# Performance work log

Measured on AMD Instinct MI355X. Metric: run time of the kernel, lower is better.

Reference implementation:

```python
import jax, jax.numpy as jnp
import numpy as np


def setup_inputs() -> dict:
    key = jax.random.key(0)
    k1, k2, k3, k4 = jax.random.split(key, 4)
    B, N, F, S, OUT = 8, 50000, 32, 16, 64
    x = jax.random.normal(k1, (B, N, F), dtype=jnp.float32)
    spiral_adj = jax.random.randint(k2, (B, N, S), 0, N, dtype=jnp.int64)
    W = jax.random.normal(k3, (OUT, F * S), dtype=jnp.float32) * (1.0 / np.sqrt(F * S))
    b = jax.random.normal(k4, (OUT,), dtype=jnp.float32) * 0.01
    return {"x": x, "spiral_adj": spiral_adj, "W": W, "b": b}


def reference(x, spiral_adj, W, b):
    B, N, F = x.shape
    S = spiral_adj.shape[-1]
    # Per-batch gather of spiral neighbors: (B, N, S, F)
    spirals = jax.vmap(lambda xb, ab: xb[ab])(x, spiral_adj)
    spirals = spirals.reshape(B, N, S * F)
    # Linear: y = spirals @ W^T + b, then ELU
    out = jnp.einsum('bnk,ok->bno', spirals, W) + b
    out = jax.nn.elu(out)
    # zero out the last (padding) vertex
    mask = jnp.ones((1, N, 1), dtype=out.dtype).at[0, -1, 0].set(0.0)
    return out * mask
```

## Files before the change

kernel.cpp:

```cpp
#include <hip/hip_runtime.h>
#include <hip/hip_bf16.h>
#include <string.h>

#define B_ 8
#define N_ 50000
#define F_ 32
#define S_ 16
#define O_ 64
#define K_ (F_ * S_)
#define XELEMS (B_ * N_ * F_)
#define TPB (N_ / 16)
#define BPB 196

typedef __attribute__((ext_vector_type(8))) short bf16x8;
typedef __attribute__((ext_vector_type(4))) float f32x4;
typedef __attribute__((ext_vector_type(4))) int int4v;

union bfpack { bf16x8 v; __hip_bfloat16 h[8]; };

__global__ __launch_bounds__(256) void prep_kernel(const float* __restrict__ W,
                                                   unsigned short* __restrict__ Wb,
                                                   const float* __restrict__ x,
                                                   unsigned short* __restrict__ xb) {
    int bid = blockIdx.x;
    if (bid < 128) {
        int i = bid * 256 + threadIdx.x;
        int j = i & 7;
        int o = (i >> 3) & 63;
        int qk = i >> 9;
        int quad = qk & 3;
        int kt = qk >> 2;
        __hip_bfloat16 h = __float2bfloat16(W[o * K_ + kt * 32 + quad * 8 + j]);
        unsigned short u; memcpy(&u, &h, 2);
        Wb[i] = u;
    } else {
        int i = (bid - 128) * 256 + threadIdx.x;
        if (i < XELEMS / 8) {
            size_t base = (size_t)i * 8;
            f32x4 a = __builtin_nontemporal_load((const f32x4*)(x + base));
            f32x4 b = __builtin_nontemporal_load((const f32x4*)(x + base + 4));
            bfpack p;
            p.h[0] = __float2bfloat16(a[0]); p.h[1] = __float2bfloat16(a[1]);
            p.h[2] = __float2bfloat16(a[2]); p.h[3] = __float2bfloat16(a[3]);
            p.h[4] = __float2bfloat16(b[0]); p.h[5] = __float2bfloat16(b[1]);
            p.h[6] = __float2bfloat16(b[2]); p.h[7] = __float2bfloat16(b[3]);
            *(bf16x8*)(xb + base) = p.v;
        }
    }
}

__global__ __launch_bounds__(256, 2) void spiral_kernel(
        const unsigned short* __restrict__ xb, const int* __restrict__ adj,
        const unsigned short* __restrict__ Wb, const float* __restrict__ bias,
        float* __restrict__ out) {
    const int lane = threadIdx.x & 63;
    const int wv   = threadIdx.x >> 6;
    const int m16  = lane & 15;
    const int quad = lane >> 4;

    const int b  = blockIdx.x & 7;
    const int jb = blockIdx.x >> 3;
    const int tib0 = (jb * 4 + wv) * 4;

    __shared__ __align__(16) unsigned char ring[4][4][4][1024];

    int rowbase[4];
    int nn[4];
#pragma unroll
    for (int vt = 0; vt < 4; ++vt) {
        int t = tib0 + vt;
        if (t >= TPB) t = TPB - 1;
        nn[vt] = t * 16;
        rowbase[vt] = b * N_ + t * 16;
    }
    const size_t xbase = (size_t)b * N_ * F_;

    int4v aj_all[4][4];
#pragma unroll
    for (int vt = 0; vt < 4; ++vt)
#pragma unroll
        for (int kt4 = 0; kt4 < 4; ++kt4)
            aj_all[vt][kt4] = __builtin_nontemporal_load(
                (const int4v*)(adj + (size_t)(rowbase[vt] + m16) * S_ + kt4 * 4));

    f32x4 acc[4][4];
#pragma unroll
    for (int vt = 0; vt < 4; ++vt)
#pragma unroll
        for (int nt = 0; nt < 4; ++nt)
            acc[vt][nt] = (f32x4){0.f, 0.f, 0.f, 0.f};

    bf16x8 wfp[4][4];

#define GATHER_ISSUE(g_)                                                                   \
    do {                                                                                   \
        if ((g_) < 16) {                                                                   \
            const int kt4_ = (g_) >> 2, q_ = (g_) & 3;                                     \
            _Pragma("unroll")                                                              \
            for (int vt = 0; vt < 4; ++vt) {                                               \
                int a_ = aj_all[vt][kt4_][q_];                                             \
                const unsigned short* src_ = xb + xbase + (size_t)a_ * F_ + quad * 8;      \
                __builtin_amdgcn_global_load_lds(                                          \
                    (const __attribute__((address_space(1))) void*)src_,                   \
                    (__attribute__((address_space(3))) void*)&ring[wv][(g_) & 3][vt][0],   \
                    16, 0, 0);                                                             \
            }                                                                              \
        }                                                                                  \
    } while (0)

#define LOAD_W(g_)                                                                         \
    do {                                                                                   \
        if ((g_) < 16) {                                                                   \
            _Pragma("unroll")                                                              \
            for (int nt = 0; nt < 4; ++nt)                                                 \
                wfp[(g_) & 3][nt] = *(const bf16x8*)(                                      \
                    Wb + (size_t)(((g_) * 4 + quad) * 64 + nt * 16 + m16) * 8);            \
        }                                                                                  \
    } while (0)

#define SB __builtin_amdgcn_sched_barrier(0)

    GATHER_ISSUE(0); SB; LOAD_W(0); SB;
    GATHER_ISSUE(1); SB; LOAD_W(1); SB;
    GATHER_ISSUE(2); SB; LOAD_W(2); SB;

#pragma unroll
    for (int g = 0; g < 16; ++g) {
        GATHER_ISSUE(g + 3); SB;
        LOAD_W(g + 3); SB;
        if (g < 13)       asm volatile("s_waitcnt vmcnt(24)" ::: "memory");
        else if (g == 13) asm volatile("s_waitcnt vmcnt(16)" ::: "memory");
        else if (g == 14) asm volatile("s_waitcnt vmcnt(8)"  ::: "memory");
        else              asm volatile("s_waitcnt vmcnt(0)"  ::: "memory");
        SB;
        bf16x8 xf[4];
#pragma unroll
        for (int vt = 0; vt < 4; ++vt)
            xf[vt] = *(const bf16x8*)&ring[wv][g & 3][vt][(size_t)lane * 16];
#pragma unroll
        for (int vt = 0; vt < 4; ++vt)
#pragma unroll
            for (int nt = 0; nt < 4; ++nt)
                acc[vt][nt] = __builtin_amdgcn_mfma_f32_16x16x32_bf16(wfp[g & 3][nt], xf[vt], acc[vt][nt], 0, 0, 0);
        SB;
    }
#undef GATHER_ISSUE
#undef LOAD_W
#undef SB

#pragma unroll
    for (int vt = 0; vt < 4; ++vt) {
        const int n = nn[vt] + m16;
        const bool zero = (n == N_ - 1);
        float* orow = out + (size_t)(rowbase[vt] + m16) * O_ + quad * 4;
#pragma unroll
        for (int nt = 0; nt < 4; ++nt) {
            f32x4 bv = *(const f32x4*)(bias + nt * 16 + quad * 4);
            f32x4 v;
#pragma unroll
            for (int r = 0; r < 4; ++r) {
                float t = acc[vt][nt][r] + bv[r];
                t = t > 0.f ? t : (__expf(t) - 1.f);
                v[r] = zero ? 0.f : t;
            }
            *(f32x4*)(orow + nt * 16) = v;
        }
    }
}

__global__ __launch_bounds__(256) void wconv_kernel(const float* __restrict__ W,
                                                    unsigned short* __restrict__ Wb) {
    int i = blockIdx.x * 256 + threadIdx.x;
    if (i < O_ * K_) {
        int j = i & 7, o = (i >> 3) & 63, qk = i >> 9;
        int quad = qk & 3, kt = qk >> 2;
        __hip_bfloat16 h = __float2bfloat16(W[o * K_ + kt * 32 + quad * 8 + j]);
        unsigned short u; memcpy(&u, &h, 2);
        Wb[i] = u;
    }
}

__global__ __launch_bounds__(256) void spiral_f32_kernel(
        const float* __restrict__ x, const int* __restrict__ adj,
        const unsigned short* __restrict__ Wb, const float* __restrict__ bias,
        float* __restrict__ out) {
    const int lane = threadIdx.x & 63;
    const int wv = threadIdx.x >> 6;
    const int m16 = lane & 15, quad = lane >> 4;
    const int b  = blockIdx.x & 7;
    const int jb = blockIdx.x >> 3;
    const int tib0 = (jb * 4 + wv) * 4;
    int rowbase[4], nn[4];
#pragma unroll
    for (int vt = 0; vt < 4; ++vt) {
        int t = tib0 + vt;
        if (t >= TPB) t = TPB - 1;
        nn[vt] = t * 16;
        rowbase[vt] = b * N_ + t * 16;
    }
    f32x4 acc[4][4];
#pragma unroll
    for (int vt = 0; vt < 4; ++vt)
#pragma unroll
        for (int nt = 0; nt < 4; ++nt) acc[vt][nt] = (f32x4){0.f,0.f,0.f,0.f};
    for (int kt = 0; kt < 16; ++kt) {
        bf16x8 wf[4];
#pragma unroll
        for (int nt = 0; nt < 4; ++nt)
            wf[nt] = *(const bf16x8*)(Wb + (size_t)((kt * 4 + quad) * 64 + nt * 16 + m16) * 8);
#pragma unroll
        for (int vt = 0; vt < 4; ++vt) {
            int a = adj[(size_t)(rowbase[vt] + m16) * S_ + kt];
            const float* xr = x + ((size_t)b * N_ + a) * F_ + quad * 8;
            f32x4 x0 = *(const f32x4*)xr;
            f32x4 x1 = *(const f32x4*)(xr + 4);
            bfpack af;
            af.h[0]=__float2bfloat16(x0[0]); af.h[1]=__float2bfloat16(x0[1]);
            af.h[2]=__float2bfloat16(x0[2]); af.h[3]=__float2bfloat16(x0[3]);
            af.h[4]=__float2bfloat16(x1[0]); af.h[5]=__float2bfloat16(x1[1]);
            af.h[6]=__float2bfloat16(x1[2]); af.h[7]=__float2bfloat16(x1[3]);
#pragma unroll
            for (int nt = 0; nt < 4; ++nt)
                acc[vt][nt] = __builtin_amdgcn_mfma_f32_16x16x32_bf16(wf[nt], af.v, acc[vt][nt], 0, 0, 0);
        }
    }
#pragma unroll
    for (int vt = 0; vt < 4; ++vt) {
        const int n = nn[vt] + m16;
        const bool zero = (n == N_ - 1);
        float* orow = out + (size_t)(rowbase[vt] + m16) * O_ + quad * 4;
#pragma unroll
        for (int nt = 0; nt < 4; ++nt) {
            f32x4 bv = *(const f32x4*)(bias + nt * 16 + quad * 4);
            f32x4 v;
#pragma unroll
            for (int r = 0; r < 4; ++r) {
                float t = acc[vt][nt][r] + bv[r];
                t = t > 0.f ? t : (__expf(t) - 1.f);
                v[r] = zero ? 0.f : t;
            }
            *(f32x4*)(orow + nt * 16) = v;
        }
    }
}

extern "C" void kernel_launch(void* const* d_in, const int* in_sizes, int n_in,
                              void* d_out, int out_size, void* d_ws, size_t ws_size,
                              hipStream_t stream) {
    const float* x    = (const float*)d_in[0];
    const int*   adj  = (const int*)d_in[1];
    const float* W    = (const float*)d_in[2];
    const float* bias = (const float*)d_in[3];
    float* out = (float*)d_out;

    const size_t wb_bytes = (size_t)O_ * K_ * 2;
    const size_t xb_bytes = (size_t)XELEMS * 2;
    unsigned short* Wb = (unsigned short*)d_ws;
    unsigned short* xb = (unsigned short*)((char*)d_ws + wb_bytes);

    const int grid_main = 8 * BPB;

    if (ws_size >= wb_bytes + xb_bytes) {
        int grid_prep = 128 + (XELEMS / 8 + 255) / 256;
        hipLaunchKernelGGL(prep_kernel, dim3(grid_prep), dim3(256), 0, stream, W, Wb, x, xb);
        hipLaunchKernelGGL(spiral_kernel, dim3(grid_main), dim3(256), 0, stream,
                           xb, adj, Wb, bias, out);
    } else {
        hipLaunchKernelGGL(wconv_kernel, dim3(128), dim3(256), 0, stream, W, Wb);
        hipLaunchKernelGGL(spiral_f32_kernel, dim3(grid_main), dim3(256), 0, stream,
                           x, adj, Wb, bias, out);
    }
}
```

Before: 230.5 us.

## Fuse bf16 prep and spiral GEMM into persistent cooperative kernel with atomic tile queue

Merges the W/x bf16 conversion and the gather+MFMA spiral kernel into one cooperative launch of 512 blocks. A grid-wide sync separates the two phases, and blocks then pull tile indices from per-batch atomic counters instead of using a fixed grid mapping. This removes a kernel launch boundary and lets blocks balance work dynamically. In exchange it pays for a grid sync, adds atomic and __syncthreads overhead per tile, and uses fewer resident blocks (512) in the conversion phase. The counters are never reset but are offset by a base value read at kernel start.

```diff
diff --git a/kernel.cpp b/kernel.cpp
--- a/kernel.cpp
+++ b/kernel.cpp
@@ -1,4 +1,5 @@
 #include <hip/hip_runtime.h>
+#include <hip/hip_cooperative_groups.h>
 #include <hip/hip_bf16.h>
 #include <string.h>
 
@@ -11,6 +12,7 @@
 #define XELEMS (B_ * N_ * F_)
 #define TPB (N_ / 16)
 #define BPB 196
+#define GRID_COOP 512
 
 typedef __attribute__((ext_vector_type(8))) short bf16x8;
 typedef __attribute__((ext_vector_type(4))) float f32x4;
@@ -18,54 +20,13 @@
 
 union bfpack { bf16x8 v; __hip_bfloat16 h[8]; };
 
-__global__ __launch_bounds__(256) void prep_kernel(const float* __restrict__ W,
-                                                   unsigned short* __restrict__ Wb,
-                                                   const float* __restrict__ x,
-                                                   unsigned short* __restrict__ xb) {
-    int bid = blockIdx.x;
-    if (bid < 128) {
-        int i = bid * 256 + threadIdx.x;
-        int j = i & 7;
-        int o = (i >> 3) & 63;
-        int qk = i >> 9;
-        int quad = qk & 3;
-        int kt = qk >> 2;
-        __hip_bfloat16 h = __float2bfloat16(W[o * K_ + kt * 32 + quad * 8 + j]);
-        unsigned short u; memcpy(&u, &h, 2);
-        Wb[i] = u;
-    } else {
-        int i = (bid - 128) * 256 + threadIdx.x;
-        if (i < XELEMS / 8) {
-            size_t base = (size_t)i * 8;
-            f32x4 a = __builtin_nontemporal_load((const f32x4*)(x + base));
-            f32x4 b = __builtin_nontemporal_load((const f32x4*)(x + base + 4));
-            bfpack p;
-            p.h[0] = __float2bfloat16(a[0]); p.h[1] = __float2bfloat16(a[1]);
-            p.h[2] = __float2bfloat16(a[2]); p.h[3] = __float2bfloat16(a[3]);
-            p.h[4] = __float2bfloat16(b[0]); p.h[5] = __float2bfloat16(b[1]);
-            p.h[6] = __float2bfloat16(b[2]); p.h[7] = __float2bfloat16(b[3]);
-            *(bf16x8*)(xb + base) = p.v;
-        }
-    }
-}
-
-__global__ __launch_bounds__(256, 2) void spiral_kernel(
+__device__ __forceinline__ void spiral_body(
         const unsigned short* __restrict__ xb, const int* __restrict__ adj,
         const unsigned short* __restrict__ Wb, const float* __restrict__ bias,
-        float* __restrict__ out) {
-    const int lane = threadIdx.x & 63;
-    const int wv   = threadIdx.x >> 6;
-    const int m16  = lane & 15;
-    const int quad = lane >> 4;
-
-    const int b  = blockIdx.x & 7;
-    const int jb = blockIdx.x >> 3;
-    const int tib0 = (jb * 4 + wv) * 4;
-
-    __shared__ __align__(16) unsigned char ring[4][4][4][1024];
-
-    int rowbase[4];
-    int nn[4];
+        float* __restrict__ out, unsigned char* ringw,
+        int b, int tib0, int lane, int m16, int quad)
+{
+    int rowbase[4], nn[4];
 #pragma unroll
     for (int vt = 0; vt < 4; ++vt) {
         int t = tib0 + vt;
@@ -102,7 +63,7 @@
                 const unsigned short* src_ = xb + xbase + (size_t)a_ * F_ + quad * 8;      \
                 __builtin_amdgcn_global_load_lds(                                          \
                     (const __attribute__((address_space(1))) void*)src_,                   \
-                    (__attribute__((address_space(3))) void*)&ring[wv][(g_) & 3][vt][0],   \
+                    (__attribute__((address_space(3))) void*)(ringw + ((((g_) & 3) * 4 + vt) << 10)), \
                     16, 0, 0);                                                             \
             }                                                                              \
         }                                                                                  \
@@ -136,7 +97,7 @@
         bf16x8 xf[4];
 #pragma unroll
         for (int vt = 0; vt < 4; ++vt)
-            xf[vt] = *(const bf16x8*)&ring[wv][g & 3][vt][(size_t)lane * 16];
+            xf[vt] = *(const bf16x8*)(ringw + (((g & 3) * 4 + vt) << 10) + lane * 16);
 #pragma unroll
         for (int vt = 0; vt < 4; ++vt)
 #pragma unroll
@@ -166,6 +127,99 @@
             *(f32x4*)(orow + nt * 16) = v;
         }
     }
+}
+
+__global__ __launch_bounds__(256, 2) void fused_kernel(
+        const float* __restrict__ x, const int* __restrict__ adj,
+        const float* __restrict__ W, const float* __restrict__ bias,
+        float* __restrict__ out, unsigned short* __restrict__ Wb,
+        unsigned short* __restrict__ xb, unsigned int* __restrict__ ctr)
+{
+    __shared__ __align__(16) unsigned char ring[4][4][4][1024];
+    __shared__ unsigned int sh_base, sh_g;
+
+    const int tid = threadIdx.x;
+    const unsigned gid = blockIdx.x * 256u + (unsigned)tid;
+    const int b = blockIdx.x & 7;
+
+    if (tid == 0) sh_base = ctr[b];
+
+    if (gid < (unsigned)(O_ * K_)) {
+        int j = gid & 7, o = (gid >> 3) & 63, qk = gid >> 9;
+        int quad_ = qk & 3, kt = qk >> 2;
+        __hip_bfloat16 h = __float2bfloat16(W[o * K_ + kt * 32 + quad_ * 8 + j]);
+        unsigned short u; memcpy(&u, &h, 2);
+        Wb[gid] = u;
+    }
+    for (unsigned i = gid; i < (unsigned)(XELEMS / 8); i += GRID_COOP * 256u) {
+        size_t base = (size_t)i * 8;
+        f32x4 a = __builtin_nontemporal_load((const f32x4*)(x + base));
+        f32x4 c = __builtin_nontemporal_load((const f32x4*)(x + base + 4));
+        bfpack p;
+        p.h[0] = __float2bfloat16(a[0]); p.h[1] = __float2bfloat16(a[1]);
+        p.h[2] = __float2bfloat16(a[2]); p.h[3] = __float2bfloat16(a[3]);
+        p.h[4] = __float2bfloat16(c[0]); p.h[5] = __float2bfloat16(c[1]);
+        p.h[6] = __float2bfloat16(c[2]); p.h[7] = __float2bfloat16(c[3]);
+        *(bf16x8*)(xb + base) = p.v;
+    }
+    __threadfence();
+    cooperative_groups::this_grid().sync();
+
+    const int lane = tid & 63, wv = tid >> 6;
+    const int m16 = lane & 15, quad = lane >> 4;
+    unsigned char* ringw = &ring[wv][0][0][0];
+
+    for (;;) {
+        __syncthreads();
+        if (tid == 0) sh_g = atomicAdd(&ctr[b], 1u) - sh_base;
+        __syncthreads();
+        unsigned g = sh_g;
+        if (g >= (unsigned)BPB) break;
+        spiral_body(xb, adj, Wb, bias, out, ringw, b, ((int)g * 4 + wv) * 4, lane, m16, quad);
+    }
+}
+
+__global__ __launch_bounds__(256) void prep_kernel(const float* __restrict__ W,
+                                                   unsigned short* __restrict__ Wb,
+                                                   const float* __restrict__ x,
+                                                   unsigned short* __restrict__ xb) {
+    int bid = blockIdx.x;
+    if (bid < 128) {
+        int i = bid * 256 + threadIdx.x;
+        int j = i & 7, o = (i >> 3) & 63, qk = i >> 9;
+        int quad = qk & 3, kt = qk >> 2;
+        __hip_bfloat16 h = __float2bfloat16(W[o * K_ + kt * 32 + quad * 8 + j]);
+        unsigned short u; memcpy(&u, &h, 2);
+        Wb[i] = u;
+    } else {
+        int i = (bid - 128) * 256 + threadIdx.x;
+        if (i < XELEMS / 8) {
+            size_t base = (size_t)i * 8;
+            f32x4 a = __builtin_nontemporal_load((const f32x4*)(x + base));
+            f32x4 c = __builtin_nontemporal_load((const f32x4*)(x + base + 4));
+            bfpack p;
+            p.h[0] = __float2bfloat16(a[0]); p.h[1] = __float2bfloat16(a[1]);
+            p.h[2] = __float2bfloat16(a[2]); p.h[3] = __float2bfloat16(a[3]);
+            p.h[4] = __float2bfloat16(c[0]); p.h[5] = __float2bfloat16(c[1]);
+            p.h[6] = __float2bfloat16(c[2]); p.h[7] = __float2bfloat16(c[3]);
+            *(bf16x8*)(xb + base) = p.v;
+        }
+    }
+}
+
+__global__ __launch_bounds__(256, 2) void spiral_kernel(
+        const unsigned short* __restrict__ xb, const int* __restrict__ adj,
+        const unsigned short* __restrict__ Wb, const float* __restrict__ bias,
+        float* __restrict__ out) {
+    __shared__ __align__(16) unsigned char ring[4][4][4][1024];
+    const int lane = threadIdx.x & 63;
+    const int wv   = threadIdx.x >> 6;
+    const int m16  = lane & 15;
+    const int quad = lane >> 4;
+    const int b  = blockIdx.x & 7;
+    const int jb = blockIdx.x >> 3;
+    spiral_body(xb, adj, Wb, bias, out, &ring[wv][0][0][0],
+                b, (jb * 4 + wv) * 4, lane, m16, quad);
 }
 
 __global__ __launch_bounds__(256) void wconv_kernel(const float* __restrict__ W,
@@ -255,10 +309,22 @@
 
     const size_t wb_bytes = (size_t)O_ * K_ * 2;
     const size_t xb_bytes = (size_t)XELEMS * 2;
+    const size_t ctr_off  = wb_bytes + xb_bytes;
     unsigned short* Wb = (unsigned short*)d_ws;
     unsigned short* xb = (unsigned short*)((char*)d_ws + wb_bytes);
+    unsigned int*  ctr = (unsigned int*)((char*)d_ws + ctr_off);
 
     const int grid_main = 8 * BPB;
+
+    if (ws_size >= ctr_off + 32) {
+        void* args[8] = { (void*)&x, (void*)&adj, (void*)&W, (void*)&bias,
+                          (void*)&out, (void*)&Wb, (void*)&xb, (void*)&ctr };
+        hipError_t e = hipLaunchCooperativeKernel((const void*)fused_kernel,
+                                                  dim3(GRID_COOP), dim3(256),
+                                                  args, 0, stream);
+        if (e == hipSuccess) return;
+        (void)hipGetLastError();
+    }
 
     if (ws_size >= wb_bytes + xb_bytes) {
         int grid_prep = 128 + (XELEMS / 8 + 255) / 256;
```

After: 413.9 us. +79.6%, slower.

## Stage full bf16 weight matrix in LDS once per block instead of per-wave global loads

Applied to the files above, without the earlier changes.

Each block now copies the whole 64 KB bf16 weight matrix into shared memory with async global-to-LDS loads at kernel start. The MFMA loop reads weight fragments from LDS rather than issuing its own global loads, which lowers the vmcnt wait thresholds and frees registers that held the prefetched weights. In exchange, launch bounds drop to one block per CU because of the larger LDS footprint, and there is a block-wide barrier before the main loop. This cuts occupancy and the latency hiding that a second block provided.

```diff
diff --git a/kernel.cpp b/kernel.cpp
--- a/kernel.cpp
+++ b/kernel.cpp
@@ -49,10 +49,13 @@
     }
 }
 
-__global__ __launch_bounds__(256, 2) void spiral_kernel(
+__global__ __launch_bounds__(256, 1) void spiral_kernel(
         const unsigned short* __restrict__ xb, const int* __restrict__ adj,
         const unsigned short* __restrict__ Wb, const float* __restrict__ bias,
         float* __restrict__ out) {
+    __shared__ __align__(16) unsigned short Wlds[32768];
+    __shared__ __align__(16) unsigned char ring[4][4][4][1024];
+
     const int lane = threadIdx.x & 63;
     const int wv   = threadIdx.x >> 6;
     const int m16  = lane & 15;
@@ -62,10 +65,9 @@
     const int jb = blockIdx.x >> 3;
     const int tib0 = (jb * 4 + wv) * 4;
 
-    __shared__ __align__(16) unsigned char ring[4][4][4][1024];
-
-    int rowbase[4];
-    int nn[4];
+    unsigned char* ringw = &ring[wv][0][0][0];
+
+    int rowbase[4], nn[4];
 #pragma unroll
     for (int vt = 0; vt < 4; ++vt) {
         int t = tib0 + vt;
@@ -75,6 +77,18 @@
     }
     const size_t xbase = (size_t)b * N_ * F_;
 
+#define SB __builtin_amdgcn_sched_barrier(0)
+
+#pragma unroll
+    for (int i = 0; i < 16; ++i) {
+        const unsigned short* src = Wb + (((size_t)wv * 16 + i) << 9) + lane * 8;
+        __builtin_amdgcn_global_load_lds(
+            (const __attribute__((address_space(1))) void*)src,
+            (__attribute__((address_space(3))) void*)((unsigned char*)Wlds + (((wv * 16 + i)) << 10)),
+            16, 0, 0);
+    }
+    SB;
+
     int4v aj_all[4][4];
 #pragma unroll
     for (int vt = 0; vt < 4; ++vt)
@@ -82,6 +96,7 @@
         for (int kt4 = 0; kt4 < 4; ++kt4)
             aj_all[vt][kt4] = __builtin_nontemporal_load(
                 (const int4v*)(adj + (size_t)(rowbase[vt] + m16) * S_ + kt4 * 4));
+    SB;
 
     f32x4 acc[4][4];
 #pragma unroll
@@ -89,8 +104,6 @@
 #pragma unroll
         for (int nt = 0; nt < 4; ++nt)
             acc[vt][nt] = (f32x4){0.f, 0.f, 0.f, 0.f};
-
-    bf16x8 wfp[4][4];
 
 #define GATHER_ISSUE(g_)                                                                   \
     do {                                                                                   \
@@ -102,50 +115,41 @@
                 const unsigned short* src_ = xb + xbase + (size_t)a_ * F_ + quad * 8;      \
                 __builtin_amdgcn_global_load_lds(                                          \
                     (const __attribute__((address_space(1))) void*)src_,                   \
-                    (__attribute__((address_space(3))) void*)&ring[wv][(g_) & 3][vt][0],   \
+                    (__attribute__((address_space(3))) void*)(ringw + ((((g_) & 3) * 4 + vt) << 10)), \
                     16, 0, 0);                                                             \
             }                                                                              \
         }                                                                                  \
     } while (0)
 
-#define LOAD_W(g_)                                                                         \
-    do {                                                                                   \
-        if ((g_) < 16) {                                                                   \
-            _Pragma("unroll")                                                              \
-            for (int nt = 0; nt < 4; ++nt)                                                 \
-                wfp[(g_) & 3][nt] = *(const bf16x8*)(                                      \
-                    Wb + (size_t)(((g_) * 4 + quad) * 64 + nt * 16 + m16) * 8);            \
-        }                                                                                  \
-    } while (0)
-
-#define SB __builtin_amdgcn_sched_barrier(0)
-
-    GATHER_ISSUE(0); SB; LOAD_W(0); SB;
-    GATHER_ISSUE(1); SB; LOAD_W(1); SB;
-    GATHER_ISSUE(2); SB; LOAD_W(2); SB;
+    GATHER_ISSUE(0); SB;
+    GATHER_ISSUE(1); SB;
+    GATHER_ISSUE(2); SB;
+    asm volatile("s_waitcnt vmcnt(12)" ::: "memory");
+    __syncthreads();
 
 #pragma unroll
     for (int g = 0; g < 16; ++g) {
         GATHER_ISSUE(g + 3); SB;
-        LOAD_W(g + 3); SB;
-        if (g < 13)       asm volatile("s_waitcnt vmcnt(24)" ::: "memory");
-        else if (g == 13) asm volatile("s_waitcnt vmcnt(16)" ::: "memory");
-        else if (g == 14) asm volatile("s_waitcnt vmcnt(8)"  ::: "memory");
+        if (g < 13)       asm volatile("s_waitcnt vmcnt(12)" ::: "memory");
+        else if (g == 13) asm volatile("s_waitcnt vmcnt(8)"  ::: "memory");
+        else if (g == 14) asm volatile("s_waitcnt vmcnt(4)"  ::: "memory");
         else              asm volatile("s_waitcnt vmcnt(0)"  ::: "memory");
         SB;
-        bf16x8 xf[4];
+        bf16x8 xf[4], wf[4];
 #pragma unroll
         for (int vt = 0; vt < 4; ++vt)
-            xf[vt] = *(const bf16x8*)&ring[wv][g & 3][vt][(size_t)lane * 16];
+            xf[vt] = *(const bf16x8*)(ringw + (((g & 3) * 4 + vt) << 10) + lane * 16);
+#pragma unroll
+        for (int nt = 0; nt < 4; ++nt)
+            wf[nt] = *(const bf16x8*)(Wlds + (size_t)((g * 4 + quad) * 64 + nt * 16 + m16) * 8);
 #pragma unroll
         for (int vt = 0; vt < 4; ++vt)
 #pragma unroll
             for (int nt = 0; nt < 4; ++nt)
-                acc[vt][nt] = __builtin_amdgcn_mfma_f32_16x16x32_bf16(wfp[g & 3][nt], xf[vt], acc[vt][nt], 0, 0, 0);
+                acc[vt][nt] = __builtin_amdgcn_mfma_f32_16x16x32_bf16(wf[nt], xf[vt], acc[vt][nt], 0, 0, 0);
         SB;
     }
 #undef GATHER_ISSUE
-#undef LOAD_W
 #undef SB
 
 #pragma unroll
```

Result: no change. 232.8 us (+1.0%).

## Convert spiral kernel to persistent grid with per-batch atomic work counters

Applied to the files above, without the earlier changes.

Replaces the fixed 1568-block launch with 512 persistent blocks. Each block repeatedly grabs a tile index from a per-batch atomic counter, and the counters are zeroed in the prep kernel. The goal is to cut block launch and tail overhead and balance the load across CUs. In exchange it adds two barriers and an atomic per tile, and it loses the overlap of the prologue and epilogue between tiles that independent blocks had.

```diff
diff --git a/kernel.cpp b/kernel.cpp
--- a/kernel.cpp
+++ b/kernel.cpp
@@ -11,6 +11,7 @@
 #define XELEMS (B_ * N_ * F_)
 #define TPB (N_ / 16)
 #define BPB 196
+#define GRID_PERS 512
 
 typedef __attribute__((ext_vector_type(8))) short bf16x8;
 typedef __attribute__((ext_vector_type(4))) float f32x4;
@@ -21,8 +22,10 @@
 __global__ __launch_bounds__(256) void prep_kernel(const float* __restrict__ W,
                                                    unsigned short* __restrict__ Wb,
                                                    const float* __restrict__ x,
-                                                   unsigned short* __restrict__ xb) {
+                                                   unsigned short* __restrict__ xb,
+                                                   unsigned int* __restrict__ ctr) {
     int bid = blockIdx.x;
+    if (bid == 0 && threadIdx.x < 8) ctr[threadIdx.x] = 0u;
     if (bid < 128) {
         int i = bid * 256 + threadIdx.x;
         int j = i & 7;
@@ -49,23 +52,13 @@
     }
 }
 
-__global__ __launch_bounds__(256, 2) void spiral_kernel(
+__device__ __forceinline__ void spiral_body(
         const unsigned short* __restrict__ xb, const int* __restrict__ adj,
         const unsigned short* __restrict__ Wb, const float* __restrict__ bias,
-        float* __restrict__ out) {
-    const int lane = threadIdx.x & 63;
-    const int wv   = threadIdx.x >> 6;
-    const int m16  = lane & 15;
-    const int quad = lane >> 4;
-
-    const int b  = blockIdx.x & 7;
-    const int jb = blockIdx.x >> 3;
-    const int tib0 = (jb * 4 + wv) * 4;
-
-    __shared__ __align__(16) unsigned char ring[4][4][4][1024];
-
-    int rowbase[4];
-    int nn[4];
+        float* __restrict__ out, unsigned char* ringw,
+        int b, int tib0, int lane, int m16, int quad)
+{
+    int rowbase[4], nn[4];
 #pragma unroll
     for (int vt = 0; vt < 4; ++vt) {
         int t = tib0 + vt;
@@ -102,7 +95,7 @@
                 const unsigned short* src_ = xb + xbase + (size_t)a_ * F_ + quad * 8;      \
                 __builtin_amdgcn_global_load_lds(                                          \
                     (const __attribute__((address_space(1))) void*)src_,                   \
-                    (__attribute__((address_space(3))) void*)&ring[wv][(g_) & 3][vt][0],   \
+                    (__attribute__((address_space(3))) void*)(ringw + ((((g_) & 3) * 4 + vt) << 10)), \
                     16, 0, 0);                                                             \
             }                                                                              \
         }                                                                                  \
@@ -136,7 +129,7 @@
         bf16x8 xf[4];
 #pragma unroll
         for (int vt = 0; vt < 4; ++vt)
-            xf[vt] = *(const bf16x8*)&ring[wv][g & 3][vt][(size_t)lane * 16];
+            xf[vt] = *(const bf16x8*)(ringw + (((g & 3) * 4 + vt) << 10) + lane * 16);
 #pragma unroll
         for (int vt = 0; vt < 4; ++vt)
 #pragma unroll
@@ -165,6 +158,33 @@
             }
             *(f32x4*)(orow + nt * 16) = v;
         }
+    }
+}
+
+__global__ __launch_bounds__(256, 2) void spiral_kernel(
+        const unsigned short* __restrict__ xb, const int* __restrict__ adj,
+        const unsigned short* __restrict__ Wb, const float* __restrict__ bias,
+        float* __restrict__ out, unsigned int* __restrict__ ctr) {
+    __shared__ __align__(16) unsigned char ring[4][4][4][1024];
+    __shared__ unsigned int sh_g;
+
+    const int tid  = threadIdx.x;
+    const int lane = tid & 63;
+    const int wv   = tid >> 6;
+    const int m16  = lane & 15;
+    const int quad = lane >> 4;
+    const int b    = blockIdx.x & 7;
+
+    unsigned char* ringw = &ring[wv][0][0][0];
+
+    for (;;) {
+        __syncthreads();
+        if (tid == 0) sh_g = atomicAdd(&ctr[b], 1u);
+        __syncthreads();
+        const unsigned g = sh_g;
+        if (g >= (unsigned)BPB) break;
+        spiral_body(xb, adj, Wb, bias, out, ringw,
+                    b, ((int)g * 4 + wv) * 4, lane, m16, quad);
     }
 }
 
@@ -255,19 +275,20 @@
 
     const size_t wb_bytes = (size_t)O_ * K_ * 2;
     const size_t xb_bytes = (size_t)XELEMS * 2;
+    const size_t ctr_off  = wb_bytes + xb_bytes;
     unsigned short* Wb = (unsigned short*)d_ws;
     unsigned short* xb = (unsigned short*)((char*)d_ws + wb_bytes);
-
-    const int grid_main = 8 * BPB;
-
-    if (ws_size >= wb_bytes + xb_bytes) {
+    unsigned int*  ctr = (unsigned int*)((char*)d_ws + ctr_off);
+
+    if (ws_size >= ctr_off + 32) {
         int grid_prep = 128 + (XELEMS / 8 + 255) / 256;
-        hipLaunchKernelGGL(prep_kernel, dim3(grid_prep), dim3(256), 0, stream, W, Wb, x, xb);
-        hipLaunchKernelGGL(spiral_kernel, dim3(grid_main), dim3(256), 0, stream,
-                           xb, adj, Wb, bias, out);
+        hipLaunchKernelGGL(prep_kernel, dim3(grid_prep), dim3(256), 0, stream,
+                           W, Wb, x, xb, ctr);
+        hipLaunchKernelGGL(spiral_kernel, dim3(GRID_PERS), dim3(256), 0, stream,
+                           xb, adj, Wb, bias, out, ctr);
     } else {
         hipLaunchKernelGGL(wconv_kernel, dim3(128), dim3(256), 0, stream, W, Wb);
-        hipLaunchKernelGGL(spiral_f32_kernel, dim3(grid_main), dim3(256), 0, stream,
+        hipLaunchKernelGGL(spiral_f32_kernel, dim3(8 * BPB), dim3(256), 0, stream,
                            x, adj, Wb, bias, out);
     }
 }
```

After: 274.9 us. +19.3%, slower.
